# Optimization experiments

Measured on AMD Instinct MI355X. Metric: run time of the kernel, lower is better.

## Reference

```python
import jax, jax.numpy as jnp
import numpy as np

EMBED_DIM = 2048
NUM_HEADS = 32
NUM_KV_HEADS = 8
HEAD_DIM = EMBED_DIM // NUM_HEADS
KV_REPEAT = NUM_HEADS // NUM_KV_HEADS
ROPE_BASE = 10000.0


def rotate_half(x):
    # interleaved rotate: (-x_odd, x_even) re-interleaved on last dim
    x_even = x[..., ::2]
    x_odd = x[..., 1::2]
    return jnp.stack((-x_odd, x_even), axis=-1).reshape(x.shape)


def rope_cos_sin(seq_len, dtype, start_pos=0):
    inv_freq = 1.0 / (ROPE_BASE ** (jnp.arange(0, HEAD_DIM, 2, dtype=jnp.float32) / HEAD_DIM))
    pos = jnp.arange(start_pos, start_pos + seq_len, dtype=jnp.float32)
    freqs = jnp.outer(pos, inv_freq)  # [T, head_dim/2]
    cos = jnp.repeat(jnp.cos(freqs), 2, axis=-1).astype(dtype)  # [T, head_dim]
    sin = jnp.repeat(jnp.sin(freqs), 2, axis=-1).astype(dtype)
    return cos[None, None], sin[None, None]  # [1,1,T,head_dim]


def setup_inputs() -> dict:
    key = jax.random.key(0)
    ks = jax.random.split(key, 5)
    s = 0.02
    x = jax.random.normal(ks[0], (2, 2048, EMBED_DIM), dtype=jnp.float32)
    Wq = jax.random.normal(ks[1], (EMBED_DIM, EMBED_DIM), dtype=jnp.float32) * s
    Wk = jax.random.normal(ks[2], (EMBED_DIM, NUM_KV_HEADS * HEAD_DIM), dtype=jnp.float32) * s
    Wv = jax.random.normal(ks[3], (EMBED_DIM, NUM_KV_HEADS * HEAD_DIM), dtype=jnp.float32) * s
    Wo = jax.random.normal(ks[4], (EMBED_DIM, EMBED_DIM), dtype=jnp.float32) * s
    return {
        "x": x,
        "Wq": Wq, "bq": jnp.zeros((EMBED_DIM,), jnp.float32),
        "Wk": Wk, "bk": jnp.zeros((NUM_KV_HEADS * HEAD_DIM,), jnp.float32),
        "Wv": Wv, "bv": jnp.zeros((NUM_KV_HEADS * HEAD_DIM,), jnp.float32),
        "Wo": Wo, "bo": jnp.zeros((EMBED_DIM,), jnp.float32),
    }


def reference(x, Wq, bq, Wk, bk, Wv, bv, Wo, bo):
    B, T, C = x.shape
    q = (x @ Wq + bq).reshape(B, T, NUM_HEADS, HEAD_DIM).transpose(0, 2, 1, 3)      # [B,H,T,D]
    k = (x @ Wk + bk).reshape(B, T, NUM_KV_HEADS, HEAD_DIM).transpose(0, 2, 1, 3)   # [B,Hkv,T,D]
    v = (x @ Wv + bv).reshape(B, T, NUM_KV_HEADS, HEAD_DIM).transpose(0, 2, 1, 3)

    cos, sin = rope_cos_sin(T, q.dtype, start_pos=0)
    q = q * cos + rotate_half(q) * sin
    k = k * cos + rotate_half(k) * sin

    # GQA: repeat KV heads to match query heads (faithful to repeat_interleave)
    k_rep = jnp.repeat(k, KV_REPEAT, axis=1)  # [B,H,T,D]
    v_rep = jnp.repeat(v, KV_REPEAT, axis=1)

    scale = np.sqrt(HEAD_DIM).astype(np.float32)
    scores = jnp.einsum('bhqd,bhkd->bhqk', q, k_rep) / scale  # [B,H,T,T]

    # causal mask: key_pos > query_pos -> -inf
    qpos = jnp.arange(T)[:, None]
    kpos = jnp.arange(T)[None, :]
    scores = jnp.where((kpos > qpos)[None, None], -jnp.inf, scores)

    attn = jax.nn.softmax(scores, axis=-1)
    out = jnp.einsum('bhqk,bhkd->bhqd', attn, v_rep)  # [B,H,T,D]
    out = out.transpose(0, 2, 1, 3).reshape(B, T, C)
    return out @ Wo + bo
```

## Files before the change

### kernel.cpp

```cpp
#include <hip/hip_runtime.h>
#include <hip/hip_bf16.h>
#include <stdint.h>
#include <stddef.h>

#define EMBED 2048
#define TLEN  2048
#define BSZ   2
#define NH    32
#define NKV   8
#define HD    64
#define MROWS (BSZ*TLEN)
#define KVD   (NKV*HD)
#define QKVN  3072

typedef __attribute__((ext_vector_type(8))) short   s16x8;
typedef __attribute__((ext_vector_type(4))) short   s16x4;
typedef __attribute__((ext_vector_type(8))) __bf16  bf16x8;
typedef __attribute__((ext_vector_type(4))) float   f32x4;
typedef __attribute__((ext_vector_type(2))) unsigned long long u64x2;
typedef __attribute__((ext_vector_type(4))) uint32_t u32x4;

static __device__ __forceinline__ float bf2f(short u) {
  union { float f; uint32_t i; } c; c.i = ((uint32_t)(uint16_t)u) << 16; return c.f;
}
static __device__ __forceinline__ short f2bf(float f) {
  union { float f; uint32_t i; } c; c.f = f;
  uint32_t x = c.i;
  uint32_t r = (x + 0x7fffu + ((x >> 16) & 1u)) >> 16;
  return (short)(uint16_t)r;
}
static __device__ __forceinline__ bf16x8 as_bf16x8(s16x8 s) {
  return __builtin_bit_cast(bf16x8, s);
}
static __device__ __forceinline__ bf16x8 mk8(unsigned long long a, unsigned long long b) {
  u64x2 t; t.x = a; t.y = b;
  return __builtin_bit_cast(bf16x8, t);
}
static __device__ __forceinline__ bf16x8 mk8w(uint32_t w0, uint32_t w1,
                                              uint32_t w2, uint32_t w3) {
  u32x4 t; t.x = w0; t.y = w1; t.z = w2; t.w = w3;
  return __builtin_bit_cast(bf16x8, t);
}

__global__ __launch_bounds__(256) void transpose_cast_kernel(
    const float* __restrict__ W, short* __restrict__ Wt, int K, int N) {
  __shared__ float tile[32][33];
  int n0 = blockIdx.x * 32, k0 = blockIdx.y * 32;
  int tx = threadIdx.x, ty = threadIdx.y;
  #pragma unroll
  for (int i = 0; i < 32; i += 8)
    tile[ty + i][tx] = W[(size_t)(k0 + ty + i) * N + n0 + tx];
  __syncthreads();
  #pragma unroll
  for (int i = 0; i < 32; i += 8)
    Wt[(size_t)(n0 + ty + i) * K + k0 + tx] = f2bf(tile[tx][ty + i]);
}

__global__ __launch_bounds__(256) void cast_bf16_kernel(
    const float* __restrict__ in, short* __restrict__ out, int n) {
  int i = (blockIdx.x * blockDim.x + threadIdx.x) * 4;
  if (i >= n) return;
  f32x4 v = *(const f32x4*)(in + i);
  s16x4 o = { f2bf(v.x), f2bf(v.y), f2bf(v.z), f2bf(v.w) };
  *(s16x4*)(out + i) = o;
}

template<bool OUT_F32, bool TRIPLE_BIAS>
__global__ __launch_bounds__(256) void gemm_bt(
    const short* __restrict__ A, const short* __restrict__ Bt,
    const float* __restrict__ b0, const float* __restrict__ b1,
    const float* __restrict__ b2, void* __restrict__ Cout, int ldc) {
  const int K = 2048;
  __shared__ __align__(16) short As[128 * 32];
  __shared__ __align__(16) short Bs[128 * 32];
  int bn = blockIdx.x, bm = blockIdx.y;
  int tid = threadIdx.x;
  int lane = tid & 63, wave = tid >> 6;
  int wr = wave >> 1, wc = wave & 1;
  int fr = lane & 15, fk = lane >> 4;
  f32x4 acc[4][4] = {};
  const short* Ab = A + (size_t)bm * 128 * K;
  const short* Bb = Bt + (size_t)bn * 128 * K;
  for (int kt = 0; kt < K; kt += 32) {
    #pragma unroll
    for (int ii = 0; ii < 2; ++ii) {
      const int i = wave * 2 + ii;
      const int r = i * 16 + (lane >> 2);
      const int c = lane & 3;
      const size_t go = (size_t)r * K + kt + c * 8;
      __builtin_amdgcn_global_load_lds(
          (const __attribute__((address_space(1))) void*)(Ab + go),
          (__attribute__((address_space(3))) void*)&As[i * 512], 16, 0, 0);
      __builtin_amdgcn_global_load_lds(
          (const __attribute__((address_space(1))) void*)(Bb + go),
          (__attribute__((address_space(3))) void*)&Bs[i * 512], 16, 0, 0);
    }
    __syncthreads();
    bf16x8 af[4], bfr[4];
    #pragma unroll
    for (int m = 0; m < 4; ++m)
      af[m] = as_bf16x8(*(const s16x8*)&As[(wr * 64 + m * 16 + fr) * 32 + fk * 8]);
    #pragma unroll
    for (int n = 0; n < 4; ++n)
      bfr[n] = as_bf16x8(*(const s16x8*)&Bs[(wc * 64 + n * 16 + fr) * 32 + fk * 8]);
    __builtin_amdgcn_s_setprio(1);
    #pragma unroll
    for (int m = 0; m < 4; ++m)
      #pragma unroll
      for (int n = 0; n < 4; ++n)
        acc[m][n] = __builtin_amdgcn_mfma_f32_16x16x32_bf16(af[m], bfr[n], acc[m][n], 0, 0, 0);
    __builtin_amdgcn_s_setprio(0);
    __syncthreads();
  }
  int row0 = bm * 128 + wr * 64;
  int col0 = bn * 128 + wc * 64;
  #pragma unroll
  for (int n = 0; n < 4; ++n) {
    int col = col0 + n * 16 + fr;
    float bv;
    if constexpr (TRIPLE_BIAS)
      bv = (col < 2048) ? b0[col] : ((col < 2560) ? b1[col - 2048] : b2[col - 2560]);
    else
      bv = b0[col];
    #pragma unroll
    for (int m = 0; m < 4; ++m)
      #pragma unroll
      for (int j = 0; j < 4; ++j) {
        int row = row0 + m * 16 + fk * 4 + j;
        float v = acc[m][n][j] + bv;
        if constexpr (OUT_F32) ((float*)Cout)[(size_t)row * ldc + col] = v;
        else                   ((short*)Cout)[(size_t)row * ldc + col] = f2bf(v);
      }
  }
}

__global__ __launch_bounds__(256) void rope_table_kernel(float2* __restrict__ tab) {
  int idx = blockIdx.x * 256 + threadIdx.x;
  int t = idx >> 5, i = idx & 31;
  float ang = (float)t * powf(10000.0f, -(float)i / 32.0f);
  float c, s;
  sincosf(ang, &c, &s);
  tab[idx] = make_float2(c, s);
}

__global__ __launch_bounds__(256) void rope_apply_kernel(
    short* __restrict__ X, int ncols, int ldx, float oscale,
    const float2* __restrict__ tab) {
  int idx = blockIdx.x * 256 + threadIdx.x;
  int npr = ncols >> 1;
  int row = idx / npr, cp = idx - row * npr;
  int i = cp & 31;
  int t = row & (TLEN - 1);
  float2 cs = tab[(t << 5) | i];
  short* p = X + (size_t)row * ldx + cp * 2;
  float e = bf2f(p[0]), o = bf2f(p[1]);
  p[0] = f2bf((e * cs.x + o * cs.y) * oscale);
  p[1] = f2bf((o * cs.x - e * cs.y) * oscale);
}

__global__ __launch_bounds__(256) void attn_kernel(
    const short* __restrict__ Q, const short* __restrict__ Kx,
    const short* __restrict__ Vx, short* __restrict__ O) {
  const int pr = blockIdx.x;
  const int bh = blockIdx.y;
  const int b = bh >> 5, h = bh & 31, kvh = h >> 2;
  const int tid = threadIdx.x;
  const int lane = tid & 63, wave = tid >> 6;
  const int fr = lane & 15, fk = lane >> 4;

  __shared__ __align__(16) short Ks[64][72];
  __shared__ __align__(16) short VS[4 * 1040];

  const short* Kbase = Kx + (size_t)b * TLEN * QKVN + kvh * HD;
  const short* Vbase = Vx + (size_t)b * TLEN * QKVN + kvh * HD;

  const int srow = tid >> 3;
  const int scb  = (tid & 7) << 3;
  const int vd0  = scb >> 4;
  const int vco  = scb & 15;
  const unsigned trb = (unsigned)(unsigned long long)&VS[fk * 128 + fr * 4];
  const bf16x8 ones = mk8(0x3F803F803F803F80ULL, 0x3F803F803F803F80ULL);
  const int src0 = (((fk & 1) << 5) + fr) << 2;
  const int src1 = src0 + 64;
  const bool msel = (fk >> 1) != 0;

#define TRREAD(dst, OFF) asm volatile("ds_read_b64_tr_b16 %0, %1 offset:" OFF \
    : "=v"(dst) : "v"(trb) : "memory")
#define CVTPK(d, lo, hi) asm volatile("v_cvt_pk_bf16_f32 %0, %1, %2" \
    : "=v"(d) : "v"(lo), "v"(hi))

  #pragma unroll 1
  for (int rep = 0; rep < 2; ++rep) {
    const int qt = rep ? (31 - pr) : pr;
    const int q0 = qt * 64;
    const short* Qrow = Q + (size_t)(b * TLEN + q0 + wave * 16 + fr) * QKVN + h * HD;
    const bf16x8 aq0 = as_bf16x8(*(const s16x8*)&Qrow[fk * 8]);
    const bf16x8 aq1 = as_bf16x8(*(const s16x8*)&Qrow[32 + fk * 8]);
    f32x4 oacc[4] = {};
    f32x4 lacc = {};
    float m = -INFINITY;
    const int qloc = wave * 16 + fr;

    for (int kv0 = 0; kv0 <= q0; kv0 += 64) {
      #pragma unroll
      for (int it = 0; it < 2; ++it) {
        const int r = srow + it * 32;
        const size_t gro = (size_t)(kv0 + r) * QKVN + scb;
        *(s16x8*)&Ks[r][scb] = *(const s16x8*)&Kbase[gro];
        s16x8 vv = *(const s16x8*)&Vbase[gro];
        *(s16x8*)&VS[vd0 * 1040 + ((r >> 2) << 6) + ((r & 3) << 4) + vco] = vv;
      }
      __syncthreads();

      f32x4 sacc[4] = {};
      {
        bf16x8 bk0[4], bk1[4];
        #pragma unroll
        for (int mb = 0; mb < 4; ++mb) {
          bk0[mb] = as_bf16x8(*(const s16x8*)&Ks[mb * 16 + fr][fk * 8]);
          bk1[mb] = as_bf16x8(*(const s16x8*)&Ks[mb * 16 + fr][32 + fk * 8]);
        }
        __builtin_amdgcn_s_setprio(1);
        #pragma unroll
        for (int mb = 0; mb < 4; ++mb) {
          sacc[mb] = __builtin_amdgcn_mfma_f32_16x16x32_bf16(bk0[mb], aq0, sacc[mb], 0, 0, 0);
          sacc[mb] = __builtin_amdgcn_mfma_f32_16x16x32_bf16(bk1[mb], aq1, sacc[mb], 0, 0, 0);
        }
        __builtin_amdgcn_s_setprio(0);
      }

      const bool diag = (kv0 == q0);
      float sv[4][4];
      float pm = -INFINITY;
      #pragma unroll
      for (int mb = 0; mb < 4; ++mb)
        #pragma unroll
        for (int j = 0; j < 4; ++j) {
          float v = sacc[mb][j];
          if (diag && (mb * 16 + fk * 4 + j > qloc)) v = -INFINITY;
          sv[mb][j] = v;
          pm = fmaxf(pm, v);
        }
      pm = fmaxf(pm, __shfl_xor(pm, 16, 64));
      pm = fmaxf(pm, __shfl_xor(pm, 32, 64));

      if (__any(pm > m + 11.5f)) {
        const float mnew = fmaxf(m, pm);
        const float al = exp2f(m - mnew);
        m = mnew;
        lacc[0] *= al; lacc[1] *= al; lacc[2] *= al; lacc[3] *= al;
        #pragma unroll
        for (int db = 0; db < 4; ++db) {
          oacc[db][0] *= al; oacc[db][1] *= al;
          oacc[db][2] *= al; oacc[db][3] *= al;
        }
      }

      uint32_t rlo[4], rhi[4];
      #pragma unroll
      for (int mb = 0; mb < 4; ++mb) {
        float p0 = exp2f(sv[mb][0] - m);
        float p1 = exp2f(sv[mb][1] - m);
        float p2 = exp2f(sv[mb][2] - m);
        float p3 = exp2f(sv[mb][3] - m);
        CVTPK(rlo[mb], p0, p1);
        CVTPK(rhi[mb], p2, p3);
      }

      uint32_t w0, w1, w2, w3, w4, w5, w6, w7;
      {
        uint32_t a, bq_;
        a = __builtin_amdgcn_ds_bpermute(src0, (int)rlo[0]);
        bq_ = __builtin_amdgcn_ds_bpermute(src0, (int)rlo[1]);
        w0 = msel ? bq_ : a;
        a = __builtin_amdgcn_ds_bpermute(src0, (int)rhi[0]);
        bq_ = __builtin_amdgcn_ds_bpermute(src0, (int)rhi[1]);
        w1 = msel ? bq_ : a;
        a = __builtin_amdgcn_ds_bpermute(src1, (int)rlo[0]);
        bq_ = __builtin_amdgcn_ds_bpermute(src1, (int)rlo[1]);
        w2 = msel ? bq_ : a;
        a = __builtin_amdgcn_ds_bpermute(src1, (int)rhi[0]);
        bq_ = __builtin_amdgcn_ds_bpermute(src1, (int)rhi[1]);
        w3 = msel ? bq_ : a;
        a = __builtin_amdgcn_ds_bpermute(src0, (int)rlo[2]);
        bq_ = __builtin_amdgcn_ds_bpermute(src0, (int)rlo[3]);
        w4 = msel ? bq_ : a;
        a = __builtin_amdgcn_ds_bpermute(src0, (int)rhi[2]);
        bq_ = __builtin_amdgcn_ds_bpermute(src0, (int)rhi[3]);
        w5 = msel ? bq_ : a;
        a = __builtin_amdgcn_ds_bpermute(src1, (int)rlo[2]);
        bq_ = __builtin_amdgcn_ds_bpermute(src1, (int)rlo[3]);
        w6 = msel ? bq_ : a;
        a = __builtin_amdgcn_ds_bpermute(src1, (int)rhi[2]);
        bq_ = __builtin_amdgcn_ds_bpermute(src1, (int)rhi[3]);
        w7 = msel ? bq_ : a;
      }
      const bf16x8 pB0 = mk8w(w0, w1, w2, w3);
      const bf16x8 pB1 = mk8w(w4, w5, w6, w7);

      unsigned long long t00, t01, t02, t03, t10, t11, t12, t13;
      unsigned long long t20, t21, t22, t23, t30, t31, t32, t33;
      TRREAD(t00, "0");    TRREAD(t01, "128");  TRREAD(t02, "1024"); TRREAD(t03, "1152");
      TRREAD(t10, "2080"); TRREAD(t11, "2208"); TRREAD(t12, "3104"); TRREAD(t13, "3232");
      TRREAD(t20, "4160"); TRREAD(t21, "4288"); TRREAD(t22, "5184"); TRREAD(t23, "5312");
      TRREAD(t30, "6240"); TRREAD(t31, "6368"); TRREAD(t32, "7264"); TRREAD(t33, "7392");
      asm volatile("s_waitcnt lgkmcnt(0)" ::: "memory");
      __builtin_amdgcn_sched_barrier(0);
      __builtin_amdgcn_s_setprio(1);
      lacc = __builtin_amdgcn_mfma_f32_16x16x32_bf16(ones, pB0, lacc, 0, 0, 0);
      lacc = __builtin_amdgcn_mfma_f32_16x16x32_bf16(ones, pB1, lacc, 0, 0, 0);
      oacc[0] = __builtin_amdgcn_mfma_f32_16x16x32_bf16(mk8(t00, t01), pB0, oacc[0], 0, 0, 0);
      oacc[0] = __builtin_amdgcn_mfma_f32_16x16x32_bf16(mk8(t02, t03), pB1, oacc[0], 0, 0, 0);
      oacc[1] = __builtin_amdgcn_mfma_f32_16x16x32_bf16(mk8(t10, t11), pB0, oacc[1], 0, 0, 0);
      oacc[1] = __builtin_amdgcn_mfma_f32_16x16x32_bf16(mk8(t12, t13), pB1, oacc[1], 0, 0, 0);
      oacc[2] = __builtin_amdgcn_mfma_f32_16x16x32_bf16(mk8(t20, t21), pB0, oacc[2], 0, 0, 0);
      oacc[2] = __builtin_amdgcn_mfma_f32_16x16x32_bf16(mk8(t22, t23), pB1, oacc[2], 0, 0, 0);
      oacc[3] = __builtin_amdgcn_mfma_f32_16x16x32_bf16(mk8(t30, t31), pB0, oacc[3], 0, 0, 0);
      oacc[3] = __builtin_amdgcn_mfma_f32_16x16x32_bf16(mk8(t32, t33), pB1, oacc[3], 0, 0, 0);
      __builtin_amdgcn_s_setprio(0);
      __syncthreads();
    }

    {
      const float linv = 1.0f / lacc[0];
      short* orow = O + (size_t)(b * TLEN + q0 + wave * 16 + fr) * EMBED + h * HD + fk * 4;
      #pragma unroll
      for (int db = 0; db < 4; ++db) {
        s16x4 o4 = { f2bf(oacc[db][0] * linv), f2bf(oacc[db][1] * linv),
                     f2bf(oacc[db][2] * linv), f2bf(oacc[db][3] * linv) };
        *(s16x4*)&orow[db * 16] = o4;
      }
    }
  }
#undef TRREAD
#undef CVTPK
}

extern "C" void kernel_launch(void* const* d_in, const int* in_sizes, int n_in,
                              void* d_out, int out_size, void* d_ws, size_t ws_size,
                              hipStream_t stream) {
  const float* x  = (const float*)d_in[0];
  const float* Wq = (const float*)d_in[1];
  const float* bq = (const float*)d_in[2];
  const float* Wk = (const float*)d_in[3];
  const float* bk = (const float*)d_in[4];
  const float* Wv = (const float*)d_in[5];
  const float* bv = (const float*)d_in[6];
  const float* Wo = (const float*)d_in[7];
  const float* bo = (const float*)d_in[8];
  float* out = (float*)d_out;

  char* ws = (char*)d_ws;
  short* xb    = (short*)(ws);
  short* WqkvT = (short*)(ws + 16777216);
  short* WoT   = (short*)(ws + 29360128);
  short* QKV   = (short*)(ws + 37748736);
  short* Ob    = (short*)(ws);
  float2* tab  = (float2*)d_out;

  dim3 tb(32, 8);
  transpose_cast_kernel<<<dim3(EMBED / 32, EMBED / 32), tb, 0, stream>>>(Wq, WqkvT, EMBED, EMBED);
  transpose_cast_kernel<<<dim3(KVD / 32, EMBED / 32), tb, 0, stream>>>(Wk, WqkvT + (size_t)2048 * 2048, EMBED, KVD);
  transpose_cast_kernel<<<dim3(KVD / 32, EMBED / 32), tb, 0, stream>>>(Wv, WqkvT + (size_t)2560 * 2048, EMBED, KVD);
  transpose_cast_kernel<<<dim3(EMBED / 32, EMBED / 32), tb, 0, stream>>>(Wo, WoT, EMBED, EMBED);
  cast_bf16_kernel<<<(MROWS * EMBED / 4) / 256, 256, 0, stream>>>(x, xb, MROWS * EMBED);
  rope_table_kernel<<<256, 256, 0, stream>>>(tab);

  gemm_bt<false, true><<<dim3(QKVN / 128, MROWS / 128), 256, 0, stream>>>(
      xb, WqkvT, bq, bk, bv, QKV, QKVN);

  rope_apply_kernel<<<(MROWS * (EMBED / 2)) / 256, 256, 0, stream>>>(
      QKV, EMBED, QKVN, 0.125f * 1.44269504088896340736f, tab);
  rope_apply_kernel<<<(MROWS * (KVD / 2)) / 256, 256, 0, stream>>>(
      QKV + 2048, KVD, QKVN, 1.0f, tab);

  attn_kernel<<<dim3(16, BSZ * NH), 256, 0, stream>>>(
      QKV, QKV + 2048, QKV + 2560, Ob);

  gemm_bt<true, false><<<dim3(EMBED / 128, MROWS / 128), 256, 0, stream>>>(
      Ob, WoT, bo, bo, bo, out, EMBED);
}
```

Baseline: 255.9 us.

## Double-buffer V in LDS, load K directly to registers, drop bpermute shuffle

The attention inner loop now prefetches the next K tile straight from global memory into registers and the next V tile into a second LDS buffer while the current tile is computed. This replaces the per-iteration load-then-__syncthreads pattern with a single s_barrier per tile. The P-operand bpermute shuffle is removed by permuting the V row placement in LDS, so P can be packed directly from the score registers. In exchange, register pressure rises from the prefetched K fragments, and correctness depends on the new row permutation matching the MFMA operand layout.

```diff
diff --git a/kernel.cpp b/kernel.cpp
--- a/kernel.cpp
+++ b/kernel.cpp
@@ -168,8 +168,7 @@
   const int lane = tid & 63, wave = tid >> 6;
   const int fr = lane & 15, fk = lane >> 4;
 
-  __shared__ __align__(16) short Ks[64][72];
-  __shared__ __align__(16) short VS[4 * 1040];
+  __shared__ __align__(16) short VS[2 * 4160];
 
   const short* Kbase = Kx + (size_t)b * TLEN * QKVN + kvh * HD;
   const short* Vbase = Vx + (size_t)b * TLEN * QKVN + kvh * HD;
@@ -178,16 +177,18 @@
   const int scb  = (tid & 7) << 3;
   const int vd0  = scb >> 4;
   const int vco  = scb & 15;
-  const unsigned trb = (unsigned)(unsigned long long)&VS[fk * 128 + fr * 4];
+  const int p0 = (((srow >> 2) & 3) << 3) | (((srow >> 4) & 1) << 2) | (srow & 3);
+  const int vaddr0 = vd0 * 1040 + ((p0 >> 2) << 6) + ((p0 & 3) << 4) + vco;
+  const int vaddr1 = vaddr0 + 512;
+  const unsigned trbase = (unsigned)(unsigned long long)&VS[fk * 128 + fr * 4];
   const bf16x8 ones = mk8(0x3F803F803F803F80ULL, 0x3F803F803F803F80ULL);
-  const int src0 = (((fk & 1) << 5) + fr) << 2;
-  const int src1 = src0 + 64;
-  const bool msel = (fk >> 1) != 0;
 
 #define TRREAD(dst, OFF) asm volatile("ds_read_b64_tr_b16 %0, %1 offset:" OFF \
     : "=v"(dst) : "v"(trb) : "memory")
 #define CVTPK(d, lo, hi) asm volatile("v_cvt_pk_bf16_f32 %0, %1, %2" \
     : "=v"(d) : "v"(lo), "v"(hi))
+
+  bf16x8 bk0[4], bk1[4];
 
   #pragma unroll 1
   for (int rep = 0; rep < 2; ++rep) {
@@ -201,32 +202,49 @@
     float m = -INFINITY;
     const int qloc = wave * 16 + fr;
 
+    __builtin_amdgcn_s_barrier();
+    {
+      s16x8 va = *(const s16x8*)&Vbase[(size_t)srow * QKVN + scb];
+      s16x8 vb = *(const s16x8*)&Vbase[(size_t)(srow + 32) * QKVN + scb];
+      *(s16x8*)&VS[vaddr0] = va;
+      *(s16x8*)&VS[vaddr1] = vb;
+    }
+    #pragma unroll
+    for (int mb = 0; mb < 4; ++mb) {
+      const short* kp = Kbase + (size_t)(mb * 16 + fr) * QKVN + fk * 8;
+      bk0[mb] = as_bf16x8(*(const s16x8*)kp);
+      bk1[mb] = as_bf16x8(*(const s16x8*)(kp + 32));
+    }
+    asm volatile("s_waitcnt lgkmcnt(0)" ::: "memory");
+    __builtin_amdgcn_sched_barrier(0);
+
+    int cur = 0;
     for (int kv0 = 0; kv0 <= q0; kv0 += 64) {
-      #pragma unroll
-      for (int it = 0; it < 2; ++it) {
-        const int r = srow + it * 32;
-        const size_t gro = (size_t)(kv0 + r) * QKVN + scb;
-        *(s16x8*)&Ks[r][scb] = *(const s16x8*)&Kbase[gro];
-        s16x8 vv = *(const s16x8*)&Vbase[gro];
-        *(s16x8*)&VS[vd0 * 1040 + ((r >> 2) << 6) + ((r & 3) << 4) + vco] = vv;
-      }
-      __syncthreads();
+      __builtin_amdgcn_s_barrier();
+      const bool more = (kv0 + 64 <= q0);
+
+      s16x8 va, vb;
+      if (more) {
+        va = *(const s16x8*)&Vbase[(size_t)(kv0 + 64 + srow) * QKVN + scb];
+        vb = *(const s16x8*)&Vbase[(size_t)(kv0 + 64 + srow + 32) * QKVN + scb];
+      }
 
       f32x4 sacc[4] = {};
-      {
-        bf16x8 bk0[4], bk1[4];
+      __builtin_amdgcn_s_setprio(1);
+      #pragma unroll
+      for (int mb = 0; mb < 4; ++mb) {
+        sacc[mb] = __builtin_amdgcn_mfma_f32_16x16x32_bf16(bk0[mb], aq0, sacc[mb], 0, 0, 0);
+        sacc[mb] = __builtin_amdgcn_mfma_f32_16x16x32_bf16(bk1[mb], aq1, sacc[mb], 0, 0, 0);
+      }
+      __builtin_amdgcn_s_setprio(0);
+
+      if (more) {
         #pragma unroll
         for (int mb = 0; mb < 4; ++mb) {
-          bk0[mb] = as_bf16x8(*(const s16x8*)&Ks[mb * 16 + fr][fk * 8]);
-          bk1[mb] = as_bf16x8(*(const s16x8*)&Ks[mb * 16 + fr][32 + fk * 8]);
+          const short* kp = Kbase + (size_t)(kv0 + 64 + mb * 16 + fr) * QKVN + fk * 8;
+          bk0[mb] = as_bf16x8(*(const s16x8*)kp);
+          bk1[mb] = as_bf16x8(*(const s16x8*)(kp + 32));
         }
-        __builtin_amdgcn_s_setprio(1);
-        #pragma unroll
-        for (int mb = 0; mb < 4; ++mb) {
-          sacc[mb] = __builtin_amdgcn_mfma_f32_16x16x32_bf16(bk0[mb], aq0, sacc[mb], 0, 0, 0);
-          sacc[mb] = __builtin_amdgcn_mfma_f32_16x16x32_bf16(bk1[mb], aq1, sacc[mb], 0, 0, 0);
-        }
-        __builtin_amdgcn_s_setprio(0);
       }
 
       const bool diag = (kv0 == q0);
@@ -259,45 +277,22 @@
       uint32_t rlo[4], rhi[4];
       #pragma unroll
       for (int mb = 0; mb < 4; ++mb) {
-        float p0 = exp2f(sv[mb][0] - m);
-        float p1 = exp2f(sv[mb][1] - m);
-        float p2 = exp2f(sv[mb][2] - m);
-        float p3 = exp2f(sv[mb][3] - m);
-        CVTPK(rlo[mb], p0, p1);
-        CVTPK(rhi[mb], p2, p3);
-      }
-
-      uint32_t w0, w1, w2, w3, w4, w5, w6, w7;
-      {
-        uint32_t a, bq_;
-        a = __builtin_amdgcn_ds_bpermute(src0, (int)rlo[0]);
-        bq_ = __builtin_amdgcn_ds_bpermute(src0, (int)rlo[1]);
-        w0 = msel ? bq_ : a;
-        a = __builtin_amdgcn_ds_bpermute(src0, (int)rhi[0]);
-        bq_ = __builtin_amdgcn_ds_bpermute(src0, (int)rhi[1]);
-        w1 = msel ? bq_ : a;
-        a = __builtin_amdgcn_ds_bpermute(src1, (int)rlo[0]);
-        bq_ = __builtin_amdgcn_ds_bpermute(src1, (int)rlo[1]);
-        w2 = msel ? bq_ : a;
-        a = __builtin_amdgcn_ds_bpermute(src1, (int)rhi[0]);
-        bq_ = __builtin_amdgcn_ds_bpermute(src1, (int)rhi[1]);
-        w3 = msel ? bq_ : a;
-        a = __builtin_amdgcn_ds_bpermute(src0, (int)rlo[2]);
-        bq_ = __builtin_amdgcn_ds_bpermute(src0, (int)rlo[3]);
-        w4 = msel ? bq_ : a;
-        a = __builtin_amdgcn_ds_bpermute(src0, (int)rhi[2]);
-        bq_ = __builtin_amdgcn_ds_bpermute(src0, (int)rhi[3]);
-        w5 = msel ? bq_ : a;
-        a = __builtin_amdgcn_ds_bpermute(src1, (int)rlo[2]);
-        bq_ = __builtin_amdgcn_ds_bpermute(src1, (int)rlo[3]);
-        w6 = msel ? bq_ : a;
-        a = __builtin_amdgcn_ds_bpermute(src1, (int)rhi[2]);
-        bq_ = __builtin_amdgcn_ds_bpermute(src1, (int)rhi[3]);
-        w7 = msel ? bq_ : a;
-      }
-      const bf16x8 pB0 = mk8w(w0, w1, w2, w3);
-      const bf16x8 pB1 = mk8w(w4, w5, w6, w7);
-
+        float q0v = exp2f(sv[mb][0] - m);
+        float q1v = exp2f(sv[mb][1] - m);
+        float q2v = exp2f(sv[mb][2] - m);
+        float q3v = exp2f(sv[mb][3] - m);
+        CVTPK(rlo[mb], q0v, q1v);
+        CVTPK(rhi[mb], q2v, q3v);
+      }
+      const bf16x8 pB0 = mk8w(rlo[0], rhi[0], rlo[1], rhi[1]);
+      const bf16x8 pB1 = mk8w(rlo[2], rhi[2], rlo[3], rhi[3]);
+
+      if (more) {
+        *(s16x8*)&VS[(cur ^ 1) * 4160 + vaddr0] = va;
+        *(s16x8*)&VS[(cur ^ 1) * 4160 + vaddr1] = vb;
+      }
+
+      const unsigned trb = trbase + (unsigned)(cur * 8320);
       unsigned long long t00, t01, t02, t03, t10, t11, t12, t13;
       unsigned long long t20, t21, t22, t23, t30, t31, t32, t33;
       TRREAD(t00, "0");    TRREAD(t01, "128");  TRREAD(t02, "1024"); TRREAD(t03, "1152");
@@ -318,7 +313,7 @@
       oacc[3] = __builtin_amdgcn_mfma_f32_16x16x32_bf16(mk8(t30, t31), pB0, oacc[3], 0, 0, 0);
       oacc[3] = __builtin_amdgcn_mfma_f32_16x16x32_bf16(mk8(t32, t33), pB1, oacc[3], 0, 0, 0);
       __builtin_amdgcn_s_setprio(0);
-      __syncthreads();
+      cur ^= 1;
     }
 
     {
```

Result: slower. 299.4 us (+17.0%).

## Permute V shared-memory layout to drop P-matrix bpermute shuffles

Applied to the files above, without the earlier changes.

The row order in which V tiles are written to shared memory is permuted so that the P fragments produced by the QK^T MFMA already match the operand layout expected by the PV MFMA. This removes 16 ds_bpermute operations and the select logic on every KV block, freeing LDS bandwidth and VALU work in the attention inner loop. Correctness depends on the permuted V row mapping exactly matching the new P register packing order.

```diff
diff --git a/kernel.cpp b/kernel.cpp
--- a/kernel.cpp
+++ b/kernel.cpp
@@ -178,11 +178,11 @@
   const int scb  = (tid & 7) << 3;
   const int vd0  = scb >> 4;
   const int vco  = scb & 15;
+  const int p0 = (((srow >> 2) & 3) << 3) | (((srow >> 4) & 1) << 2) | (srow & 3);
+  const int vaddr0 = vd0 * 1040 + ((p0 >> 2) << 6) + ((p0 & 3) << 4) + vco;
+  const int vaddr1 = vaddr0 + 512;
   const unsigned trb = (unsigned)(unsigned long long)&VS[fk * 128 + fr * 4];
   const bf16x8 ones = mk8(0x3F803F803F803F80ULL, 0x3F803F803F803F80ULL);
-  const int src0 = (((fk & 1) << 5) + fr) << 2;
-  const int src1 = src0 + 64;
-  const bool msel = (fk >> 1) != 0;
 
 #define TRREAD(dst, OFF) asm volatile("ds_read_b64_tr_b16 %0, %1 offset:" OFF \
     : "=v"(dst) : "v"(trb) : "memory")
@@ -208,7 +208,7 @@
         const size_t gro = (size_t)(kv0 + r) * QKVN + scb;
         *(s16x8*)&Ks[r][scb] = *(const s16x8*)&Kbase[gro];
         s16x8 vv = *(const s16x8*)&Vbase[gro];
-        *(s16x8*)&VS[vd0 * 1040 + ((r >> 2) << 6) + ((r & 3) << 4) + vco] = vv;
+        *(s16x8*)&VS[it ? vaddr1 : vaddr0] = vv;
       }
       __syncthreads();
 
@@ -259,44 +259,15 @@
       uint32_t rlo[4], rhi[4];
       #pragma unroll
       for (int mb = 0; mb < 4; ++mb) {
-        float p0 = exp2f(sv[mb][0] - m);
-        float p1 = exp2f(sv[mb][1] - m);
-        float p2 = exp2f(sv[mb][2] - m);
-        float p3 = exp2f(sv[mb][3] - m);
-        CVTPK(rlo[mb], p0, p1);
-        CVTPK(rhi[mb], p2, p3);
-      }
-
-      uint32_t w0, w1, w2, w3, w4, w5, w6, w7;
-      {
-        uint32_t a, bq_;
-        a = __builtin_amdgcn_ds_bpermute(src0, (int)rlo[0]);
-        bq_ = __builtin_amdgcn_ds_bpermute(src0, (int)rlo[1]);
-        w0 = msel ? bq_ : a;
-        a = __builtin_amdgcn_ds_bpermute(src0, (int)rhi[0]);
-        bq_ = __builtin_amdgcn_ds_bpermute(src0, (int)rhi[1]);
-        w1 = msel ? bq_ : a;
-        a = __builtin_amdgcn_ds_bpermute(src1, (int)rlo[0]);
-        bq_ = __builtin_amdgcn_ds_bpermute(src1, (int)rlo[1]);
-        w2 = msel ? bq_ : a;
-        a = __builtin_amdgcn_ds_bpermute(src1, (int)rhi[0]);
-        bq_ = __builtin_amdgcn_ds_bpermute(src1, (int)rhi[1]);
-        w3 = msel ? bq_ : a;
-        a = __builtin_amdgcn_ds_bpermute(src0, (int)rlo[2]);
-        bq_ = __builtin_amdgcn_ds_bpermute(src0, (int)rlo[3]);
-        w4 = msel ? bq_ : a;
-        a = __builtin_amdgcn_ds_bpermute(src0, (int)rhi[2]);
-        bq_ = __builtin_amdgcn_ds_bpermute(src0, (int)rhi[3]);
-        w5 = msel ? bq_ : a;
-        a = __builtin_amdgcn_ds_bpermute(src1, (int)rlo[2]);
-        bq_ = __builtin_amdgcn_ds_bpermute(src1, (int)rlo[3]);
-        w6 = msel ? bq_ : a;
-        a = __builtin_amdgcn_ds_bpermute(src1, (int)rhi[2]);
-        bq_ = __builtin_amdgcn_ds_bpermute(src1, (int)rhi[3]);
-        w7 = msel ? bq_ : a;
-      }
-      const bf16x8 pB0 = mk8w(w0, w1, w2, w3);
-      const bf16x8 pB1 = mk8w(w4, w5, w6, w7);
+        float e0 = exp2f(sv[mb][0] - m);
+        float e1 = exp2f(sv[mb][1] - m);
+        float e2 = exp2f(sv[mb][2] - m);
+        float e3 = exp2f(sv[mb][3] - m);
+        CVTPK(rlo[mb], e0, e1);
+        CVTPK(rhi[mb], e2, e3);
+      }
+      const bf16x8 pB0 = mk8w(rlo[0], rhi[0], rlo[1], rhi[1]);
+      const bf16x8 pB1 = mk8w(rlo[2], rhi[2], rlo[3], rhi[3]);
 
       unsigned long long t00, t01, t02, t03, t10, t11, t12, t13;
       unsigned long long t20, t21, t22, t23, t30, t31, t32, t33;
```

New measurement: 242.6 us. -5.2%, faster.
